# Kernel optimization log

Measured on AMD Instinct MI355X. Metric: run time of the kernel, lower is better.

Reference implementation:

```python
import jax, jax.numpy as jnp
import numpy as np

N_NODES = 50000
N_EDGES = 800000
N_GRAPHS = 512
IN_CH, HID_CH, OUT_CH, N_CLASSES = 128, 64, 64, 10


def gcn_conv(x, src, dst, ew, W, b, n_nodes):
    """PyG GCNConv: add self-loops (weight 1), symmetric normalization, x @ W, scatter-add at dst, + bias."""
    xw = x @ W  # [N, out]
    loop = jnp.arange(n_nodes, dtype=src.dtype)
    src_f = jnp.concatenate([src, loop])
    dst_f = jnp.concatenate([dst, loop])
    ew_f = jnp.concatenate([ew, jnp.ones((n_nodes,), dtype=ew.dtype)])
    deg = jax.ops.segment_sum(ew_f, dst_f, num_segments=n_nodes)  # [N]
    dinv = jnp.where(deg > 0, jax.lax.rsqrt(deg), 0.0)
    norm = dinv[src_f] * ew_f * dinv[dst_f]  # [E+N]
    msg = norm[:, None] * xw[src_f]  # gather + scale
    out = jax.ops.segment_sum(msg, dst_f, num_segments=n_nodes)  # scatter-add
    return out + b


def setup_inputs() -> dict:
    key = jax.random.key(0)
    ks = jax.random.split(key, 12)
    x = jax.random.normal(ks[0], (N_NODES, IN_CH), dtype=jnp.float32)
    edge_index = jax.random.randint(ks[1], (2, N_EDGES), 0, N_NODES, dtype=jnp.int64)
    edge_attr = jax.random.uniform(ks[2], (N_EDGES,), dtype=jnp.float32)
    batch = jnp.sort(jax.random.randint(ks[3], (N_NODES,), 0, N_GRAPHS, dtype=jnp.int64))
    def glorot(k, shape):
        lim = np.sqrt(6.0 / (shape[0] + shape[1]))
        return jax.random.uniform(k, shape, jnp.float32, -lim, lim)
    W1 = glorot(ks[4], (IN_CH, HID_CH))
    b1 = jnp.zeros((HID_CH,), jnp.float32)
    W2 = glorot(ks[5], (HID_CH, OUT_CH))
    b2 = jnp.zeros((OUT_CH,), jnp.float32)
    LW1 = glorot(ks[6], (OUT_CH, 32))
    Lb1 = jnp.zeros((32,), jnp.float32)
    LW2 = glorot(ks[7], (32, N_CLASSES))
    Lb2 = jnp.zeros((N_CLASSES,), jnp.float32)
    return {"x": x, "edge_index": edge_index, "edge_attr": edge_attr, "batch": batch,
            "W1": W1, "b1": b1, "W2": W2, "b2": b2,
            "LW1": LW1, "Lb1": Lb1, "LW2": LW2, "Lb2": Lb2}


def reference(x, edge_index, edge_attr, batch, W1, b1, W2, b2, LW1, Lb1, LW2, Lb2):
    src, dst = edge_index[0], edge_index[1]
    h = gcn_conv(x, src, dst, edge_attr, W1, b1, N_NODES)
    h = jax.nn.relu(h)
    h = gcn_conv(h, src, dst, edge_attr, W2, b2, N_NODES)
    # global mean pool over graphs
    sums = jax.ops.segment_sum(h, batch, num_segments=N_GRAPHS)  # [G, OUT]
    cnt = jax.ops.segment_sum(jnp.ones((N_NODES,), h.dtype), batch, num_segments=N_GRAPHS)
    pooled = sums / jnp.maximum(cnt, 1.0)[:, None]
    # head (dropout treated as identity for deterministic reference)
    h1 = pooled @ LW1 + Lb1
    return h1 @ LW2 + Lb2
```

## Files before the change

kernel.cpp:

```cpp
#include <hip/hip_runtime.h>
#include <hip/hip_bf16.h>

static constexpr int NN = 50000;
static constexpr int NE = 800000;
static constexpr int NG = 512;
static constexpr int NB = 196;
static constexpr int GEMM_BLOCKS = (NN + 63) / 64;
static constexpr int HB = 240;

__device__ __forceinline__ float bfu(ushort u) {
    return __uint_as_float((unsigned)u << 16);
}
__device__ __forceinline__ ushort fbf(float f) {
    return __hip_bfloat16_raw(__float2bfloat16(f)).x;
}


__global__ void zero_kernel(float* __restrict__ p, int n) {
    int i = blockIdx.x * blockDim.x + threadIdx.x;
    if (i < n) p[i] = 0.f;
}

template <int K, bool BF16IN>
__device__ __forceinline__ void gemm_body(const void* __restrict__ Xv,
                                          const float* __restrict__ W,
                                          ushort* __restrict__ out,
                                          int row0, float Xs[][68], float Ws[][64]) {
    int tx = threadIdx.x & 15, ty = threadIdx.x >> 4;
    float acc[4][4] = {};
    for (int kb = 0; kb < K; kb += 64) {
        __syncthreads();
        for (int i = threadIdx.x; i < 1024; i += 256) {
            int kk = i >> 4, c4 = i & 15;
            *(float4*)&Ws[kk][c4 * 4] = *(const float4*)&W[(kb + kk) * 64 + c4 * 4];
        }
        if constexpr (BF16IN) {
            const ushort* X = (const ushort*)Xv;
            for (int i = threadIdx.x; i < 512; i += 256) {
                int r = i >> 3, g = i & 7;
                int gr = row0 + r; if (gr >= NN) gr = NN - 1;
                uint4 v = *(const uint4*)(X + (long long)gr * K + kb + g * 8);
                float4 f0, f1;
                f0.x = __uint_as_float(v.x << 16); f0.y = __uint_as_float(v.x & 0xffff0000u);
                f0.z = __uint_as_float(v.y << 16); f0.w = __uint_as_float(v.y & 0xffff0000u);
                f1.x = __uint_as_float(v.z << 16); f1.y = __uint_as_float(v.z & 0xffff0000u);
                f1.z = __uint_as_float(v.w << 16); f1.w = __uint_as_float(v.w & 0xffff0000u);
                *(float4*)&Xs[r][g * 8] = f0;
                *(float4*)&Xs[r][g * 8 + 4] = f1;
            }
        } else {
            const float* X = (const float*)Xv;
            for (int i = threadIdx.x; i < 1024; i += 256) {
                int r = i >> 4, k4 = i & 15;
                int gr = row0 + r; if (gr >= NN) gr = NN - 1;
                float4 v = *(const float4*)(X + (long long)gr * K + kb + k4 * 4);
                *(float4*)&Xs[r][k4 * 4] = v;
            }
        }
        __syncthreads();
#pragma unroll
        for (int k4 = 0; k4 < 16; ++k4) {
            float4 w0 = *(const float4*)&Ws[k4 * 4 + 0][tx * 4];
            float4 w1 = *(const float4*)&Ws[k4 * 4 + 1][tx * 4];
            float4 w2 = *(const float4*)&Ws[k4 * 4 + 2][tx * 4];
            float4 w3 = *(const float4*)&Ws[k4 * 4 + 3][tx * 4];
            float4 x0 = *(const float4*)&Xs[ty * 4 + 0][k4 * 4];
            float4 x1 = *(const float4*)&Xs[ty * 4 + 1][k4 * 4];
            float4 x2 = *(const float4*)&Xs[ty * 4 + 2][k4 * 4];
            float4 x3 = *(const float4*)&Xs[ty * 4 + 3][k4 * 4];
#define GCN_ROW(j, xv) \
            acc[j][0]=fmaf(xv.x,w0.x,acc[j][0]); acc[j][1]=fmaf(xv.x,w0.y,acc[j][1]); \
            acc[j][2]=fmaf(xv.x,w0.z,acc[j][2]); acc[j][3]=fmaf(xv.x,w0.w,acc[j][3]); \
            acc[j][0]=fmaf(xv.y,w1.x,acc[j][0]); acc[j][1]=fmaf(xv.y,w1.y,acc[j][1]); \
            acc[j][2]=fmaf(xv.y,w1.z,acc[j][2]); acc[j][3]=fmaf(xv.y,w1.w,acc[j][3]); \
            acc[j][0]=fmaf(xv.z,w2.x,acc[j][0]); acc[j][1]=fmaf(xv.z,w2.y,acc[j][1]); \
            acc[j][2]=fmaf(xv.z,w2.z,acc[j][2]); acc[j][3]=fmaf(xv.z,w2.w,acc[j][3]); \
            acc[j][0]=fmaf(xv.w,w3.x,acc[j][0]); acc[j][1]=fmaf(xv.w,w3.y,acc[j][1]); \
            acc[j][2]=fmaf(xv.w,w3.z,acc[j][2]); acc[j][3]=fmaf(xv.w,w3.w,acc[j][3]);
            GCN_ROW(0, x0)
            GCN_ROW(1, x1)
            GCN_ROW(2, x2)
            GCN_ROW(3, x3)
#undef GCN_ROW
        }
    }
#pragma unroll
    for (int j = 0; j < 4; ++j) {
        int r = row0 + ty * 4 + j;
        if (r < NN) {
            ushort4 sv;
            sv.x = fbf(acc[j][0]); sv.y = fbf(acc[j][1]);
            sv.z = fbf(acc[j][2]); sv.w = fbf(acc[j][3]);
            *(ushort4*)(out + (long long)r * 64 + tx * 4) = sv;
        }
    }
}

__global__ __launch_bounds__(256) void hist_gemm_kernel(const int* __restrict__ dst,
                                                        const float* __restrict__ ew,
                                                        unsigned long long* __restrict__ hA,
                                                        unsigned long long* __restrict__ hB,
                                                        int* __restrict__ rank,
                                                        const float* __restrict__ X,
                                                        const float* __restrict__ W,
                                                        ushort* __restrict__ out) {
    __shared__ float Xs[64][68];
    __shared__ float Ws[64][64];
    if (blockIdx.x < HB) {
        const int T = HB * 256;
        int tid = blockIdx.x * 256 + threadIdx.x;
        unsigned long long* tab = (tid & 1) ? hB : hA;
        for (int e = tid; e < NE; e += 2 * T) {
            int e1 = e + T;
            bool has1 = e1 < NE;
            int d0 = dst[e];
            float v0 = ew[e];
            int d1 = has1 ? dst[e1] : 0;
            float v1 = has1 ? ew[e1] : 0.f;
            unsigned long long p0 = (1ULL << 40) |
                (unsigned long long)__float2uint_rn(v0 * 1048576.0f);
            unsigned long long p1 = (1ULL << 40) |
                (unsigned long long)__float2uint_rn(v1 * 1048576.0f);
            unsigned long long o0 = atomicAdd(&tab[d0], p0);
            unsigned long long o1 = 0;
            if (has1) o1 = atomicAdd(&tab[d1], p1);
            rank[e] = (int)(o0 >> 40);
            if (has1) rank[e1] = (int)(o1 >> 40);
        }
        return;
    }
    gemm_body<128, false>(X, W, out, (blockIdx.x - HB) * 64, Xs, Ws);
}

template <int K, bool BF16IN>
__global__ __launch_bounds__(256) void gemm_kernel(const void* __restrict__ Xv,
                                                   const float* __restrict__ W,
                                                   ushort* __restrict__ out) {
    __shared__ float Xs[64][68];
    __shared__ float Ws[64][64];
    gemm_body<K, BF16IN>(Xv, W, out, blockIdx.x * 64, Xs, Ws);
}

__global__ __launch_bounds__(256) void dinv_scanA_kernel(const unsigned long long* __restrict__ hA,
                                                         const unsigned long long* __restrict__ hB,
                                                         float* __restrict__ dinv,
                                                         int* __restrict__ partial) {
    int i = blockIdx.x * 256 + threadIdx.x;
    int cnt = 0;
    if (i < NN) {
        unsigned long long va = hA[i], vb = hB[i];
        constexpr unsigned long long M = (1ULL << 40) - 1;
        cnt = (int)(va >> 40) + (int)(vb >> 40);
        float deg = (float)((va & M) + (vb & M)) * (1.0f / 1048576.0f) + 1.0f;
        dinv[i] = 1.0f / sqrtf(deg);
    }
    __shared__ int wsum[4];
    int lane = threadIdx.x & 63, wid = threadIdx.x >> 6;
    int v = cnt;
#pragma unroll
    for (int off = 32; off > 0; off >>= 1) v += __shfl_down(v, (unsigned)off, 64);
    if (lane == 0) wsum[wid] = v;
    __syncthreads();
    if (threadIdx.x == 0) partial[blockIdx.x] = wsum[0] + wsum[1] + wsum[2] + wsum[3];
}

__device__ __forceinline__ int block_scan_inclusive(int v, int* wtot) {
    int lane = threadIdx.x & 63, wid = threadIdx.x >> 6;
    int inc = v;
#pragma unroll
    for (int off = 1; off < 64; off <<= 1) {
        int n = __shfl_up(inc, (unsigned)off, 64);
        if (lane >= off) inc += n;
    }
    if (lane == 63) wtot[wid] = inc;
    __syncthreads();
    int add = 0;
    for (int w = 0; w < wid; ++w) add += wtot[w];
    return inc + add;
}

__global__ __launch_bounds__(256) void scanC_bounds_kernel(const unsigned long long* __restrict__ hA,
                                                           const unsigned long long* __restrict__ hB,
                                                           const int* __restrict__ partial,
                                                           int* __restrict__ rowptr,
                                                           const int* __restrict__ batch,
                                                           int* __restrict__ gbeg,
                                                           int* __restrict__ gend) {
    __shared__ int wtot[4];
    __shared__ int poff_s;
    int t = threadIdx.x;
    if (t < 64) {
        int s = 0;
        for (int i = t; i < (int)blockIdx.x; i += 64) s += partial[i];
#pragma unroll
        for (int off = 32; off > 0; off >>= 1) s += __shfl_down(s, (unsigned)off, 64);
        if (t == 0) poff_s = s;
    }
    int i = blockIdx.x * 256 + t;
    int v = 0;
    if (i < NN) v = (int)(hA[i] >> 40) + (int)(hB[i] >> 40);
    int incl = block_scan_inclusive(v, wtot);
    if (i < NN) {
        rowptr[i + 1] = poff_s + incl;
        int g = batch[i];
        if (i == 0 || batch[i - 1] != g) gbeg[g] = i;
        if (i == NN - 1 || batch[i + 1] != g) gend[g] = i + 1;
    }
    if (i == 0) rowptr[0] = 0;
}

__global__ __launch_bounds__(256) void scatter_kernel(const int* __restrict__ src,
                                                      const int* __restrict__ dst,
                                                      const float* __restrict__ ew,
                                                      const float* __restrict__ dinv,
                                                      const int* __restrict__ rowptr,
                                                      const int* __restrict__ rank,
                                                      const unsigned long long* __restrict__ hA,
                                                      int2* __restrict__ epack) {
    int e = blockIdx.x * blockDim.x + threadIdx.x;
    if (e >= NE) return;
    int s = src[e], d = dst[e];
    int pos = rowptr[d] + rank[e];
    if (e & 1) pos += (int)(hA[d] >> 40);
    float coef = dinv[s] * ew[e];
    epack[pos] = make_int2(s, __float_as_int(coef));
}

template <bool RELU>
__global__ __launch_bounds__(256) void agg_kernel(const ushort* __restrict__ xw,
                                                  const int* __restrict__ rowptr,
                                                  const int2* __restrict__ epack,
                                                  const float* __restrict__ dinv,
                                                  const float* __restrict__ bias,
                                                  ushort* __restrict__ out) {
    int node = blockIdx.x * 4 + (threadIdx.x >> 6);
    if (node >= NN) return;
    int lane = threadIdx.x & 63;
    int e8 = lane >> 3;
    int l8 = lane & 7;
    int beg = rowptr[node], end = rowptr[node + 1];
    float a0 = 0.f, a1 = 0.f, a2 = 0.f, a3 = 0.f;
    float a4 = 0.f, a5 = 0.f, a6 = 0.f, a7 = 0.f;
    for (int j = beg + e8; j < end; j += 8) {
        int2 p = epack[j];
        uint4 v = *(const uint4*)(xw + p.x * 64 + l8 * 8);
        float w = __int_as_float(p.y);
        a0 = fmaf(w, __uint_as_float(v.x << 16), a0);
        a1 = fmaf(w, __uint_as_float(v.x & 0xffff0000u), a1);
        a2 = fmaf(w, __uint_as_float(v.y << 16), a2);
        a3 = fmaf(w, __uint_as_float(v.y & 0xffff0000u), a3);
        a4 = fmaf(w, __uint_as_float(v.z << 16), a4);
        a5 = fmaf(w, __uint_as_float(v.z & 0xffff0000u), a5);
        a6 = fmaf(w, __uint_as_float(v.w << 16), a6);
        a7 = fmaf(w, __uint_as_float(v.w & 0xffff0000u), a7);
    }
#define RED(x) x += __shfl_xor(x, 8); x += __shfl_xor(x, 16); x += __shfl_xor(x, 32);
    RED(a0) RED(a1) RED(a2) RED(a3) RED(a4) RED(a5) RED(a6) RED(a7)
#undef RED
    if (e8 == 0) {
        float di = dinv[node];
        float d2 = di * di;
        uint4 us = *(const uint4*)(xw + node * 64 + l8 * 8);
        float4 bv0 = *(const float4*)(bias + l8 * 8);
        float4 bv1 = *(const float4*)(bias + l8 * 8 + 4);
        float o0 = fmaf(di, a0, fmaf(d2, __uint_as_float(us.x << 16), bv0.x));
        float o1 = fmaf(di, a1, fmaf(d2, __uint_as_float(us.x & 0xffff0000u), bv0.y));
        float o2 = fmaf(di, a2, fmaf(d2, __uint_as_float(us.y << 16), bv0.z));
        float o3 = fmaf(di, a3, fmaf(d2, __uint_as_float(us.y & 0xffff0000u), bv0.w));
        float o4 = fmaf(di, a4, fmaf(d2, __uint_as_float(us.z << 16), bv1.x));
        float o5 = fmaf(di, a5, fmaf(d2, __uint_as_float(us.z & 0xffff0000u), bv1.y));
        float o6 = fmaf(di, a6, fmaf(d2, __uint_as_float(us.w << 16), bv1.z));
        float o7 = fmaf(di, a7, fmaf(d2, __uint_as_float(us.w & 0xffff0000u), bv1.w));
        if (RELU) {
            o0 = fmaxf(o0, 0.f); o1 = fmaxf(o1, 0.f); o2 = fmaxf(o2, 0.f); o3 = fmaxf(o3, 0.f);
            o4 = fmaxf(o4, 0.f); o5 = fmaxf(o5, 0.f); o6 = fmaxf(o6, 0.f); o7 = fmaxf(o7, 0.f);
        }
        uint4 sv;
        sv.x = (unsigned)fbf(o0) | ((unsigned)fbf(o1) << 16);
        sv.y = (unsigned)fbf(o2) | ((unsigned)fbf(o3) << 16);
        sv.z = (unsigned)fbf(o4) | ((unsigned)fbf(o5) << 16);
        sv.w = (unsigned)fbf(o6) | ((unsigned)fbf(o7) << 16);
        *(uint4*)(out + node * 64 + l8 * 8) = sv;
    }
}

__global__ __launch_bounds__(256) void poolhead_kernel(const ushort* __restrict__ h,
                                                       const int* __restrict__ gbeg,
                                                       const int* __restrict__ gend,
                                                       const float* __restrict__ LW1,
                                                       const float* __restrict__ Lb1,
                                                       const float* __restrict__ LW2,
                                                       const float* __restrict__ Lb2,
                                                       float* __restrict__ out) {
    __shared__ float pp[4][64];
    __shared__ float p[64];
    __shared__ float t1[32];
    int g = blockIdx.x, t = threadIdx.x;
    int lane = t & 63, wid = t >> 6;
    int b = gbeg[g], e = gend[g];
    float acc = 0.f;
    for (int i = b + wid; i < e; i += 4) acc += bfu(h[i * 64 + lane]);
    pp[wid][lane] = acc;
    __syncthreads();
    if (t < 64) {
        float s = pp[0][t] + pp[1][t] + pp[2][t] + pp[3][t];
        p[t] = s / fmaxf((float)(e - b), 1.0f);
    }
    __syncthreads();
    if (t < 32) {
        float a = Lb1[t];
#pragma unroll
        for (int k = 0; k < 64; ++k) a = fmaf(p[k], LW1[k * 32 + t], a);
        t1[t] = a;
    }
    __syncthreads();
    if (t < 10) {
        float a = Lb2[t];
#pragma unroll
        for (int j = 0; j < 32; ++j) a = fmaf(t1[j], LW2[j * 10 + t], a);
        out[g * 10 + t] = a;
    }
}


extern "C" void kernel_launch(void* const* d_in, const int* in_sizes, int n_in,
                              void* d_out, int out_size, void* d_ws, size_t ws_size,
                              hipStream_t stream) {
    const float* x     = (const float*)d_in[0];
    const int*   ei    = (const int*)d_in[1];
    const float* ew    = (const float*)d_in[2];
    const int*   batch = (const int*)d_in[3];
    const float* W1    = (const float*)d_in[4];
    const float* b1    = (const float*)d_in[5];
    const float* W2    = (const float*)d_in[6];
    const float* b2    = (const float*)d_in[7];
    const float* LW1   = (const float*)d_in[8];
    const float* Lb1   = (const float*)d_in[9];
    const float* LW2   = (const float*)d_in[10];
    const float* Lb2   = (const float*)d_in[11];

    const int* src = ei;
    const int* dst = ei + NE;

    float* ws = (float*)d_ws;
    unsigned long long* hA = (unsigned long long*)ws;
    unsigned long long* hB = (unsigned long long*)(ws + 100096);
    int*   gbeg   = (int*)(ws + 200192);
    int*   gend   = (int*)(ws + 200704);
    float* dinv   = ws + 201216;
    int*   rowptr = (int*)(ws + 251264);
    int*   partial= (int*)(ws + 301344);
    int2*  epack  = (int2*)(ws + 301568);
    ushort* xwA   = (ushort*)(ws + 1901568);
    ushort* h12   = (ushort*)(ws + 3501568);
    int*   rank   = (int*)(ws + 5101568);

    zero_kernel<<<(201216 + 255) / 256, 256, 0, stream>>>(ws, 201216);

    hist_gemm_kernel<<<HB + GEMM_BLOCKS, 256, 0, stream>>>(dst, ew, hA, hB, rank,
                                                           x, W1, xwA);
    dinv_scanA_kernel<<<NB, 256, 0, stream>>>(hA, hB, dinv, partial);
    scanC_bounds_kernel<<<NB, 256, 0, stream>>>(hA, hB, partial, rowptr, batch, gbeg, gend);
    scatter_kernel<<<(NE + 255) / 256, 256, 0, stream>>>(src, dst, ew, dinv, rowptr,
                                                         rank, hA, epack);

    agg_kernel<true><<<(NN + 3) / 4, 256, 0, stream>>>(xwA, rowptr, epack, dinv, b1, h12);

    gemm_kernel<64, true><<<GEMM_BLOCKS, 256, 0, stream>>>(h12, W2, xwA);
    agg_kernel<false><<<(NN + 3) / 4, 256, 0, stream>>>(xwA, rowptr, epack, dinv, b2, h12);

    poolhead_kernel<<<NG, 256, 0, stream>>>(h12, gbeg, gend, LW1, Lb1, LW2, Lb2, (float*)d_out);
}
```

Measured before the change: 247.9 us.

## Fuse layer-1 aggregation with second GEMM and use single degree histogram

Layer-1 aggregation now feeds its ReLU output through shared memory straight into the second 64x64 weight multiply in the same kernel, so the separate GEMM launch and the bf16 round trip of the hidden activations are gone. The degree histogram moves from two split tables to one 64-bit atomic table, with fewer histogram blocks, which simplifies the scan and scatter and shrinks the zeroing pass. The cost is more atomic contention on the single table, plus a per-block W2 load into shared memory and a small scalar matvec per node. The hidden layer also skips its bf16 rounding before the GEMM, which changes numerics slightly.

```diff
diff --git a/kernel.cpp b/kernel.cpp
--- a/kernel.cpp
+++ b/kernel.cpp
@@ -6,7 +6,8 @@
 static constexpr int NG = 512;
 static constexpr int NB = 196;
 static constexpr int GEMM_BLOCKS = (NN + 63) / 64;
-static constexpr int HB = 240;
+static constexpr int HB = 128;
+static_assert(NN % 4 == 0, "agg kernels assume exact 4-node blocks");
 
 __device__ __forceinline__ float bfu(ushort u) {
     return __uint_as_float((unsigned)u << 16);
@@ -21,8 +22,8 @@
     if (i < n) p[i] = 0.f;
 }
 
-template <int K, bool BF16IN>
-__device__ __forceinline__ void gemm_body(const void* __restrict__ Xv,
+template <int K>
+__device__ __forceinline__ void gemm_body(const float* __restrict__ X,
                                           const float* __restrict__ W,
                                           ushort* __restrict__ out,
                                           int row0, float Xs[][68], float Ws[][64]) {
@@ -34,28 +35,11 @@
             int kk = i >> 4, c4 = i & 15;
             *(float4*)&Ws[kk][c4 * 4] = *(const float4*)&W[(kb + kk) * 64 + c4 * 4];
         }
-        if constexpr (BF16IN) {
-            const ushort* X = (const ushort*)Xv;
-            for (int i = threadIdx.x; i < 512; i += 256) {
-                int r = i >> 3, g = i & 7;
-                int gr = row0 + r; if (gr >= NN) gr = NN - 1;
-                uint4 v = *(const uint4*)(X + (long long)gr * K + kb + g * 8);
-                float4 f0, f1;
-                f0.x = __uint_as_float(v.x << 16); f0.y = __uint_as_float(v.x & 0xffff0000u);
-                f0.z = __uint_as_float(v.y << 16); f0.w = __uint_as_float(v.y & 0xffff0000u);
-                f1.x = __uint_as_float(v.z << 16); f1.y = __uint_as_float(v.z & 0xffff0000u);
-                f1.z = __uint_as_float(v.w << 16); f1.w = __uint_as_float(v.w & 0xffff0000u);
-                *(float4*)&Xs[r][g * 8] = f0;
-                *(float4*)&Xs[r][g * 8 + 4] = f1;
-            }
-        } else {
-            const float* X = (const float*)Xv;
-            for (int i = threadIdx.x; i < 1024; i += 256) {
-                int r = i >> 4, k4 = i & 15;
-                int gr = row0 + r; if (gr >= NN) gr = NN - 1;
-                float4 v = *(const float4*)(X + (long long)gr * K + kb + k4 * 4);
-                *(float4*)&Xs[r][k4 * 4] = v;
-            }
+        for (int i = threadIdx.x; i < 1024; i += 256) {
+            int r = i >> 4, k4 = i & 15;
+            int gr = row0 + r; if (gr >= NN) gr = NN - 1;
+            float4 v = *(const float4*)(X + (long long)gr * K + kb + k4 * 4);
+            *(float4*)&Xs[r][k4 * 4] = v;
         }
         __syncthreads();
 #pragma unroll
@@ -98,8 +82,7 @@
 
 __global__ __launch_bounds__(256) void hist_gemm_kernel(const int* __restrict__ dst,
                                                         const float* __restrict__ ew,
-                                                        unsigned long long* __restrict__ hA,
-                                                        unsigned long long* __restrict__ hB,
+                                                        unsigned long long* __restrict__ h,
                                                         int* __restrict__ rank,
                                                         const float* __restrict__ X,
                                                         const float* __restrict__ W,
@@ -107,51 +90,27 @@
     __shared__ float Xs[64][68];
     __shared__ float Ws[64][64];
     if (blockIdx.x < HB) {
-        const int T = HB * 256;
-        int tid = blockIdx.x * 256 + threadIdx.x;
-        unsigned long long* tab = (tid & 1) ? hB : hA;
-        for (int e = tid; e < NE; e += 2 * T) {
-            int e1 = e + T;
-            bool has1 = e1 < NE;
-            int d0 = dst[e];
-            float v0 = ew[e];
-            int d1 = has1 ? dst[e1] : 0;
-            float v1 = has1 ? ew[e1] : 0.f;
-            unsigned long long p0 = (1ULL << 40) |
-                (unsigned long long)__float2uint_rn(v0 * 1048576.0f);
-            unsigned long long p1 = (1ULL << 40) |
-                (unsigned long long)__float2uint_rn(v1 * 1048576.0f);
-            unsigned long long o0 = atomicAdd(&tab[d0], p0);
-            unsigned long long o1 = 0;
-            if (has1) o1 = atomicAdd(&tab[d1], p1);
-            rank[e] = (int)(o0 >> 40);
-            if (has1) rank[e1] = (int)(o1 >> 40);
+        for (int e = blockIdx.x * 256 + threadIdx.x; e < NE; e += HB * 256) {
+            int d = dst[e];
+            unsigned int fx = __float2uint_rn(ew[e] * 1048576.0f);
+            unsigned long long pack = (1ULL << 40) | (unsigned long long)fx;
+            unsigned long long old = atomicAdd(&h[d], pack);
+            rank[e] = (int)(old >> 40);
         }
         return;
     }
-    gemm_body<128, false>(X, W, out, (blockIdx.x - HB) * 64, Xs, Ws);
-}
-
-template <int K, bool BF16IN>
-__global__ __launch_bounds__(256) void gemm_kernel(const void* __restrict__ Xv,
-                                                   const float* __restrict__ W,
-                                                   ushort* __restrict__ out) {
-    __shared__ float Xs[64][68];
-    __shared__ float Ws[64][64];
-    gemm_body<K, BF16IN>(Xv, W, out, blockIdx.x * 64, Xs, Ws);
-}
-
-__global__ __launch_bounds__(256) void dinv_scanA_kernel(const unsigned long long* __restrict__ hA,
-                                                         const unsigned long long* __restrict__ hB,
+    gemm_body<128>(X, W, out, (blockIdx.x - HB) * 64, Xs, Ws);
+}
+
+__global__ __launch_bounds__(256) void dinv_scanA_kernel(const unsigned long long* __restrict__ h,
                                                          float* __restrict__ dinv,
                                                          int* __restrict__ partial) {
     int i = blockIdx.x * 256 + threadIdx.x;
     int cnt = 0;
     if (i < NN) {
-        unsigned long long va = hA[i], vb = hB[i];
-        constexpr unsigned long long M = (1ULL << 40) - 1;
-        cnt = (int)(va >> 40) + (int)(vb >> 40);
-        float deg = (float)((va & M) + (vb & M)) * (1.0f / 1048576.0f) + 1.0f;
+        unsigned long long v = h[i];
+        cnt = (int)(v >> 40);
+        float deg = (float)(v & ((1ULL << 40) - 1)) * (1.0f / 1048576.0f) + 1.0f;
         dinv[i] = 1.0f / sqrtf(deg);
     }
     __shared__ int wsum[4];
@@ -179,8 +138,7 @@
     return inc + add;
 }
 
-__global__ __launch_bounds__(256) void scanC_bounds_kernel(const unsigned long long* __restrict__ hA,
-                                                           const unsigned long long* __restrict__ hB,
+__global__ __launch_bounds__(256) void scanC_bounds_kernel(const unsigned long long* __restrict__ h,
                                                            const int* __restrict__ partial,
                                                            int* __restrict__ rowptr,
                                                            const int* __restrict__ batch,
@@ -197,8 +155,7 @@
         if (t == 0) poff_s = s;
     }
     int i = blockIdx.x * 256 + t;
-    int v = 0;
-    if (i < NN) v = (int)(hA[i] >> 40) + (int)(hB[i] >> 40);
+    int v = (i < NN) ? (int)(h[i] >> 40) : 0;
     int incl = block_scan_inclusive(v, wtot);
     if (i < NN) {
         rowptr[i + 1] = poff_s + incl;
@@ -215,15 +172,75 @@
                                                       const float* __restrict__ dinv,
                                                       const int* __restrict__ rowptr,
                                                       const int* __restrict__ rank,
-                                                      const unsigned long long* __restrict__ hA,
                                                       int2* __restrict__ epack) {
     int e = blockIdx.x * blockDim.x + threadIdx.x;
     if (e >= NE) return;
     int s = src[e], d = dst[e];
     int pos = rowptr[d] + rank[e];
-    if (e & 1) pos += (int)(hA[d] >> 40);
     float coef = dinv[s] * ew[e];
     epack[pos] = make_int2(s, __float_as_int(coef));
+}
+
+__global__ __launch_bounds__(256) void agg_gemm_kernel(const ushort* __restrict__ xw,
+                                                       const int* __restrict__ rowptr,
+                                                       const int2* __restrict__ epack,
+                                                       const float* __restrict__ dinv,
+                                                       const float* __restrict__ bias,
+                                                       const float* __restrict__ W2,
+                                                       ushort* __restrict__ xw2) {
+    __shared__ float W2s[64][64];
+    __shared__ float h1s[4][64];
+    for (int i = threadIdx.x; i < 1024; i += 256)
+        ((float4*)W2s)[i] = ((const float4*)W2)[i];
+    int w = threadIdx.x >> 6;
+    int node = blockIdx.x * 4 + w;
+    int lane = threadIdx.x & 63;
+    int e8 = lane >> 3;
+    int l8 = lane & 7;
+    int beg = rowptr[node], end = rowptr[node + 1];
+    float a0 = 0.f, a1 = 0.f, a2 = 0.f, a3 = 0.f;
+    float a4 = 0.f, a5 = 0.f, a6 = 0.f, a7 = 0.f;
+    for (int j = beg + e8; j < end; j += 8) {
+        int2 p = epack[j];
+        uint4 v = *(const uint4*)(xw + p.x * 64 + l8 * 8);
+        float wt = __int_as_float(p.y);
+        a0 = fmaf(wt, __uint_as_float(v.x << 16), a0);
+        a1 = fmaf(wt, __uint_as_float(v.x & 0xffff0000u), a1);
+        a2 = fmaf(wt, __uint_as_float(v.y << 16), a2);
+        a3 = fmaf(wt, __uint_as_float(v.y & 0xffff0000u), a3);
+        a4 = fmaf(wt, __uint_as_float(v.z << 16), a4);
+        a5 = fmaf(wt, __uint_as_float(v.z & 0xffff0000u), a5);
+        a6 = fmaf(wt, __uint_as_float(v.w << 16), a6);
+        a7 = fmaf(wt, __uint_as_float(v.w & 0xffff0000u), a7);
+    }
+#define RED(x) x += __shfl_xor(x, 8); x += __shfl_xor(x, 16); x += __shfl_xor(x, 32);
+    RED(a0) RED(a1) RED(a2) RED(a3) RED(a4) RED(a5) RED(a6) RED(a7)
+#undef RED
+    if (e8 == 0) {
+        float di = dinv[node];
+        float d2 = di * di;
+        uint4 us = *(const uint4*)(xw + node * 64 + l8 * 8);
+        float4 bv0 = *(const float4*)(bias + l8 * 8);
+        float4 bv1 = *(const float4*)(bias + l8 * 8 + 4);
+        float o0 = fmaf(di, a0, fmaf(d2, __uint_as_float(us.x << 16), bv0.x));
+        float o1 = fmaf(di, a1, fmaf(d2, __uint_as_float(us.x & 0xffff0000u), bv0.y));
+        float o2 = fmaf(di, a2, fmaf(d2, __uint_as_float(us.y << 16), bv0.z));
+        float o3 = fmaf(di, a3, fmaf(d2, __uint_as_float(us.y & 0xffff0000u), bv0.w));
+        float o4 = fmaf(di, a4, fmaf(d2, __uint_as_float(us.z << 16), bv1.x));
+        float o5 = fmaf(di, a5, fmaf(d2, __uint_as_float(us.z & 0xffff0000u), bv1.y));
+        float o6 = fmaf(di, a6, fmaf(d2, __uint_as_float(us.w << 16), bv1.z));
+        float o7 = fmaf(di, a7, fmaf(d2, __uint_as_float(us.w & 0xffff0000u), bv1.w));
+        *(float4*)&h1s[w][l8 * 8]     = make_float4(fmaxf(o0, 0.f), fmaxf(o1, 0.f),
+                                                    fmaxf(o2, 0.f), fmaxf(o3, 0.f));
+        *(float4*)&h1s[w][l8 * 8 + 4] = make_float4(fmaxf(o4, 0.f), fmaxf(o5, 0.f),
+                                                    fmaxf(o6, 0.f), fmaxf(o7, 0.f));
+    }
+    __syncthreads();
+    int outch = lane;
+    float acc = 0.f;
+#pragma unroll
+    for (int k = 0; k < 64; ++k) acc = fmaf(h1s[w][k], W2s[k][outch], acc);
+    xw2[node * 64 + outch] = fbf(acc);
 }
 
 template <bool RELU>
@@ -234,7 +251,6 @@
                                                   const float* __restrict__ bias,
                                                   ushort* __restrict__ out) {
     int node = blockIdx.x * 4 + (threadIdx.x >> 6);
-    if (node >= NN) return;
     int lane = threadIdx.x & 63;
     int e8 = lane >> 3;
     int l8 = lane & 7;
@@ -343,31 +359,29 @@
     const int* dst = ei + NE;
 
     float* ws = (float*)d_ws;
-    unsigned long long* hA = (unsigned long long*)ws;
-    unsigned long long* hB = (unsigned long long*)(ws + 100096);
-    int*   gbeg   = (int*)(ws + 200192);
-    int*   gend   = (int*)(ws + 200704);
-    float* dinv   = ws + 201216;
-    int*   rowptr = (int*)(ws + 251264);
-    int*   partial= (int*)(ws + 301344);
-    int2*  epack  = (int2*)(ws + 301568);
-    ushort* xwA   = (ushort*)(ws + 1901568);
-    ushort* h12   = (ushort*)(ws + 3501568);
-    int*   rank   = (int*)(ws + 5101568);
-
-    zero_kernel<<<(201216 + 255) / 256, 256, 0, stream>>>(ws, 201216);
-
-    hist_gemm_kernel<<<HB + GEMM_BLOCKS, 256, 0, stream>>>(dst, ew, hA, hB, rank,
-                                                           x, W1, xwA);
-    dinv_scanA_kernel<<<NB, 256, 0, stream>>>(hA, hB, dinv, partial);
-    scanC_bounds_kernel<<<NB, 256, 0, stream>>>(hA, hB, partial, rowptr, batch, gbeg, gend);
+    unsigned long long* h64 = (unsigned long long*)ws;
+    int*   gbeg   = (int*)(ws + 100096);
+    int*   gend   = (int*)(ws + 100608);
+    float* dinv   = ws + 101120;
+    int*   rowptr = (int*)(ws + 151168);
+    int*   partial= (int*)(ws + 201248);
+    int2*  epack  = (int2*)(ws + 201504);
+    ushort* xwA   = (ushort*)(ws + 1801504);
+    ushort* xwB   = (ushort*)(ws + 3401504);
+    int*   rank   = (int*)(ws + 5001504);
+    ushort* h2    = xwA;
+
+    zero_kernel<<<(101120 + 255) / 256, 256, 0, stream>>>(ws, 101120);
+
+    hist_gemm_kernel<<<HB + GEMM_BLOCKS, 256, 0, stream>>>(dst, ew, h64, rank, x, W1, xwA);
+    dinv_scanA_kernel<<<NB, 256, 0, stream>>>(h64, dinv, partial);
+    scanC_bounds_kernel<<<NB, 256, 0, stream>>>(h64, partial, rowptr, batch, gbeg, gend);
     scatter_kernel<<<(NE + 255) / 256, 256, 0, stream>>>(src, dst, ew, dinv, rowptr,
-                                                         rank, hA, epack);
-
-    agg_kernel<true><<<(NN + 3) / 4, 256, 0, stream>>>(xwA, rowptr, epack, dinv, b1, h12);
-
-    gemm_kernel<64, true><<<GEMM_BLOCKS, 256, 0, stream>>>(h12, W2, xwA);
-    agg_kernel<false><<<(NN + 3) / 4, 256, 0, stream>>>(xwA, rowptr, epack, dinv, b2, h12);
-
-    poolhead_kernel<<<NG, 256, 0, stream>>>(h12, gbeg, gend, LW1, Lb1, LW2, Lb2, (float*)d_out);
-}
+                                                         rank, epack);
+
+    agg_gemm_kernel<<<NN / 4, 256, 0, stream>>>(xwA, rowptr, epack, dinv, b1, W2, xwB);
+
+    agg_kernel<false><<<NN / 4, 256, 0, stream>>>(xwB, rowptr, epack, dinv, b2, h2);
+
+    poolhead_kernel<<<NG, 256, 0, stream>>>(h2, gbeg, gend, LW1, Lb1, LW2, Lb2, (float*)d_out);
+}
```

After: 230.7 us. 7.0% less time.
